# Performance work log

Hardware: AMD Instinct MI355X
Metric: run time of the kernel (lower is better)

## Reference

```python
import jax, jax.numpy as jnp
import numpy as np

EPS = 1e-06

def rmsnorm(x, w):
    x32 = x.astype(jnp.float32)
    var = jnp.mean(x32 * x32, axis=-1, keepdims=True)
    return w * (x32 * jax.lax.rsqrt(var + EPS)).astype(x.dtype)

def setup_inputs() -> dict:
    B, T, C = 16, 256, 16
    token_dim, text_dim = 1024, 512
    key = jax.random.key(0)
    ks = jax.random.split(key, 8)
    token_embeds = jax.random.normal(ks[0], (B, T, token_dim), dtype=jnp.float32)
    char_embeds = jax.random.normal(ks[1], (B, T, C, text_dim), dtype=jnp.float32)
    filler_embed = jax.random.normal(ks[2], (text_dim,), dtype=jnp.float32)
    mask = jax.random.randint(ks[3], (B, T, C), 0, 2).astype(bool)
    mask = mask.at[0].set(True)  # force max valid count == T*C (static output shape)
    token_ids_mask = jnp.ones((B, T), dtype=bool)
    # xavier-uniform-ish weights
    def xav(k, fan_out, fan_in, gain=1.0):
        lim = gain * np.sqrt(6.0 / (fan_in + fan_out))
        return jax.random.uniform(k, (fan_out, fan_in), jnp.float32, -lim, lim)
    W_down = xav(ks[4], text_dim, token_dim)
    W_proj = xav(ks[5], 3, text_dim, gain=0.2)
    W_fusion = xav(ks[6], text_dim, text_dim)
    w_pre = jnp.ones((token_dim,), jnp.float32)
    w_tok = jnp.ones((text_dim,), jnp.float32)
    w_char = jnp.ones((text_dim,), jnp.float32)
    return {"token_embeds": token_embeds, "token_ids_mask": token_ids_mask,
            "char_embeds": char_embeds, "char_ids_mask": mask,
            "filler_embed": filler_embed, "w_pre": w_pre, "w_tok": w_tok,
            "w_char": w_char, "W_down": W_down, "W_proj": W_proj,
            "W_fusion": W_fusion, "max_valid_chars": T * C}

def reference(token_embeds, token_ids_mask, char_embeds, char_ids_mask,
              filler_embed, w_pre, w_tok, w_char, W_down, W_proj, W_fusion,
              max_valid_chars):
    B, T, C, d = char_embeds.shape
    MV = int(max_valid_chars)
    tok = rmsnorm(token_embeds, w_pre)                       # [B,T,token_dim]
    feats = rmsnorm(jnp.einsum('btk,dk->btd', tok, W_down), w_tok)  # [B,T,d]
    params = jnp.einsum('btd,pd->btp', jax.nn.silu(feats), W_proj)  # [B,T,3]
    scale = params[..., 0][:, :, None, None]                 # [B,T,1,1]
    shift = params[..., 1][:, :, None, None]
    gate = jax.nn.sigmoid(params[..., 2][:, :, None, None])
    cn = rmsnorm(char_embeds, w_char)                        # [B,T,C,d]
    fused = jnp.einsum('btcd,ed->btce', jax.nn.silu(cn * (1.0 + scale) + shift), W_fusion)
    fused = gate * fused + (1.0 - gate) * cn                 # [B,T,C,d]
    flat = fused.reshape(B, T * C, d)
    m = char_ids_mask.reshape(B, T * C).astype(jnp.int32)
    pos = jnp.cumsum(m, axis=1) - 1                          # dest within row
    offs = jnp.arange(B, dtype=jnp.int32)[:, None] * MV
    idx = jnp.where(m > 0, offs + pos, B * MV)               # invalid -> dump slot
    buf = jnp.broadcast_to(filler_embed, (B * MV + 1, d))
    buf = buf.at[idx.reshape(-1)].set(flat.reshape(-1, d))
    return buf[: B * MV].reshape(B, MV, d)
```

## Files before the change

### kernel.cpp

```cpp
#include <hip/hip_runtime.h>
#include <cstdint>
#include <cstddef>

#define EPS 1e-6f

typedef short bf16x8 __attribute__((ext_vector_type(8)));
typedef float f32x4  __attribute__((ext_vector_type(4)));

__device__ __forceinline__ short f2bf(float x) {
    uint32_t u = __builtin_bit_cast(uint32_t, x);
    return (short)((u + 0x7FFFu + ((u >> 16) & 1u)) >> 16);
}

__global__ __launch_bounds__(256) void k_front(
    const void* __restrict__ maskp, int* __restrict__ v_list, int* __restrict__ counts,
    const float* __restrict__ Wf, short* __restrict__ Wfbf,
    const float* __restrict__ Wd, short* __restrict__ Wdbf,
    const float* __restrict__ tokens, const float* __restrict__ w_pre,
    short* __restrict__ tokbf) {
    const int blk = blockIdx.x, tid = threadIdx.x;
    if (blk < 16) {
        __shared__ int wtot[4], woff[4];
        __shared__ int mode_s;
        const int b = blk, lane = tid & 63, wave = tid >> 6;
        if (tid == 0) mode_s = 0;
        __syncthreads();
        {
            int bad = 0;
#pragma unroll
            for (int q = 0; q < 4; ++q)
                bad |= (((const uint32_t*)maskp)[q * 256 + tid] > 1u) ? 1 : 0;
            if (bad) mode_s = 1;
        }
        __syncthreads();
        int f[16];
        if (mode_s) {
            const uint4 v = ((const uint4*)maskp)[(b << 8) + tid];
            const uint32_t ws[4] = {v.x, v.y, v.z, v.w};
#pragma unroll
            for (int q = 0; q < 4; ++q) {
                f[q * 4 + 0] = (ws[q] & 0x000000ffu) != 0;
                f[q * 4 + 1] = (ws[q] & 0x0000ff00u) != 0;
                f[q * 4 + 2] = (ws[q] & 0x00ff0000u) != 0;
                f[q * 4 + 3] = (ws[q] & 0xff000000u) != 0;
            }
        } else {
            const uint4* mp = (const uint4*)maskp + ((size_t)b << 10) + tid * 4;
#pragma unroll
            for (int q = 0; q < 4; ++q) {
                const uint4 v = mp[q];
                f[q * 4 + 0] = v.x != 0; f[q * 4 + 1] = v.y != 0;
                f[q * 4 + 2] = v.z != 0; f[q * 4 + 3] = v.w != 0;
            }
        }
        int c = 0;
#pragma unroll
        for (int q = 0; q < 16; ++q) c += f[q];
        int incl = c;
#pragma unroll
        for (int off = 1; off < 64; off <<= 1) {
            const int n = __shfl_up(incl, off);
            if (lane >= off) incl += n;
        }
        if (lane == 63) wtot[wave] = incl;
        __syncthreads();
        if (tid == 0) {
            int run = 0;
#pragma unroll
            for (int wv = 0; wv < 4; ++wv) { woff[wv] = run; run += wtot[wv]; }
            counts[b] = run;
        }
        __syncthreads();
        int base = woff[wave] + incl - c;
        int* vl = v_list + (b << 12);
        const int i0 = tid * 16;
#pragma unroll
        for (int q = 0; q < 16; ++q)
            if (f[q]) vl[base++] = i0 + q;
    } else if (blk < 784) {
        const int gid = (blk - 16) * 256 + tid;
        const float* s; short* d; int i;
        if (gid < 65536) { s = Wf; d = Wfbf; i = gid; }
        else             { s = Wd; d = Wdbf; i = gid - 65536; }
        const float4 v = ((const float4*)s)[i];
        short4 o;
        o.x = f2bf(v.x); o.y = f2bf(v.y); o.z = f2bf(v.z); o.w = f2bf(v.w);
        ((short4*)d)[i] = o;
    } else {
        const int lane = tid & 63, wave = tid >> 6;
        const int row = (blk - 784) * 4 + wave;
        const float* xp = tokens + (size_t)row * 1024 + lane * 16;
        float4 x[4];
#pragma unroll
        for (int q = 0; q < 4; ++q) x[q] = *(const float4*)&xp[q * 4];
        float ss = 0.f;
#pragma unroll
        for (int q = 0; q < 4; ++q)
            ss += x[q].x * x[q].x + x[q].y * x[q].y + x[q].z * x[q].z + x[q].w * x[q].w;
#pragma unroll
        for (int off = 32; off > 0; off >>= 1) ss += __shfl_down(ss, off);
        ss = __shfl(ss, 0);
        const float r = rsqrtf(ss * (1.0f / 1024.0f) + EPS);
        const float* wp = w_pre + lane * 16;
        short* op = tokbf + (size_t)row * 1024 + lane * 16;
#pragma unroll
        for (int h = 0; h < 2; ++h) {
            bf16x8 o;
#pragma unroll
            for (int q = 0; q < 2; ++q) {
                const float4 wv = *(const float4*)&wp[h * 8 + q * 4];
                const float4 xv = x[h * 2 + q];
                o[q * 4 + 0] = f2bf(xv.x * wv.x * r);
                o[q * 4 + 1] = f2bf(xv.y * wv.y * r);
                o[q * 4 + 2] = f2bf(xv.z * wv.z * r);
                o[q * 4 + 3] = f2bf(xv.w * wv.w * r);
            }
            *(bf16x8*)&op[h * 8] = o;
        }
    }
}

__global__ __launch_bounds__(256) void k_gemm_tok(const short* __restrict__ tokbf,
                                                  const short* __restrict__ Wdbf,
                                                  float* __restrict__ feats) {
    __shared__ short As[128 * 32];
    __shared__ short Bs[128 * 32];
    const int tid = threadIdx.x, lane = tid & 63, w = tid >> 6;
    const int kt = blockIdx.x >> 7;
    const int mt = (blockIdx.x >> 2) & 31, nt = blockIdx.x & 3;
    const int wm = w >> 1, wn = w & 1;
    const int kbase = kt * 512;
    const short* hA = tokbf + (size_t)mt * 128 * 1024;
    const short* wB = Wdbf + (size_t)nt * 128 * 1024;

    f32x4 acc[4][4];
#pragma unroll
    for (int mi = 0; mi < 4; ++mi)
#pragma unroll
        for (int ni = 0; ni < 4; ++ni) acc[mi][ni] = (f32x4)0.f;

    const int rA = lane & 15, ch = lane >> 4;
    for (int kk = 0; kk < 512; kk += 32) {
#pragma unroll
        for (int q = 0; q < 2; ++q) {
            const int cid = (w * 2 + q) * 64 + lane;
            const int r = cid >> 2, kc = cid & 3;
            const int kcs = kc ^ ((r >> 1) & 3);
            const size_t go = (size_t)r * 1024 + kbase + kk + kcs * 8;
            __builtin_amdgcn_global_load_lds(
                (const __attribute__((address_space(1))) uint32_t*)(hA + go),
                (__attribute__((address_space(3))) uint32_t*)&As[(w * 2 + q) * 512], 16, 0, 0);
            __builtin_amdgcn_global_load_lds(
                (const __attribute__((address_space(1))) uint32_t*)(wB + go),
                (__attribute__((address_space(3))) uint32_t*)&Bs[(w * 2 + q) * 512], 16, 0, 0);
        }
        __syncthreads();
        bf16x8 af[4], bfr[4];
#pragma unroll
        for (int mi = 0; mi < 4; ++mi) {
            const int row = wm * 64 + mi * 16 + rA;
            af[mi] = *(const bf16x8*)&As[row * 32 + ((ch ^ ((row >> 1) & 3)) << 3)];
        }
#pragma unroll
        for (int ni = 0; ni < 4; ++ni) {
            const int row = wn * 64 + ni * 16 + rA;
            bfr[ni] = *(const bf16x8*)&Bs[row * 32 + ((ch ^ ((row >> 1) & 3)) << 3)];
        }
#pragma unroll
        for (int mi = 0; mi < 4; ++mi)
#pragma unroll
            for (int ni = 0; ni < 4; ++ni)
                acc[mi][ni] = __builtin_amdgcn_mfma_f32_16x16x32_bf16(af[mi], bfr[ni], acc[mi][ni], 0, 0, 0);
        __syncthreads();
    }
    float* fo = feats + (size_t)kt * 4096 * 512;
    const int rowb = mt * 128 + wm * 64 + (lane >> 4) * 4;
    const int colb = nt * 128 + wn * 64 + (lane & 15);
#pragma unroll
    for (int mi = 0; mi < 4; ++mi)
#pragma unroll
        for (int ni = 0; ni < 4; ++ni)
#pragma unroll
            for (int rg = 0; rg < 4; ++rg)
                fo[(size_t)(rowb + mi * 16 + rg) * 512 + colb + ni * 16] = acc[mi][ni][rg];
}

__global__ __launch_bounds__(64) void k_params(
    const float* __restrict__ feats_pre, const float* __restrict__ w_tok,
    const float* __restrict__ W_proj, float* __restrict__ params) {
    const int tk = blockIdx.x;
    const int lane = threadIdx.x;
    const int d0 = lane * 8;
    const float* fp0 = feats_pre + (size_t)tk * 512 + d0;
    const float* fp1 = fp0 + (size_t)4096 * 512;
    const float4 a0 = *(const float4*)&fp0[0];
    const float4 a1 = *(const float4*)&fp0[4];
    const float4 b0 = *(const float4*)&fp1[0];
    const float4 b1 = *(const float4*)&fp1[4];
    const float4 f0 = make_float4(a0.x + b0.x, a0.y + b0.y, a0.z + b0.z, a0.w + b0.w);
    const float4 f1 = make_float4(a1.x + b1.x, a1.y + b1.y, a1.z + b1.z, a1.w + b1.w);
    float ss = f0.x * f0.x + f0.y * f0.y + f0.z * f0.z + f0.w * f0.w
             + f1.x * f1.x + f1.y * f1.y + f1.z * f1.z + f1.w * f1.w;
#pragma unroll
    for (int off = 32; off > 0; off >>= 1) ss += __shfl_down(ss, off);
    ss = __shfl(ss, 0);
    const float rms = rsqrtf(ss * (1.0f / 512.0f) + EPS);

    const float4 wt0 = *(const float4*)&w_tok[d0];
    const float4 wt1 = *(const float4*)&w_tok[d0 + 4];
    float fv[8] = {f0.x, f0.y, f0.z, f0.w, f1.x, f1.y, f1.z, f1.w};
    float wv[8] = {wt0.x, wt0.y, wt0.z, wt0.w, wt1.x, wt1.y, wt1.z, wt1.w};
    float s[8];
#pragma unroll
    for (int j = 0; j < 8; ++j) {
        const float v = fv[j] * wv[j] * rms;
        s[j] = v / (1.0f + expf(-v));
    }
    float p[3];
#pragma unroll
    for (int q = 0; q < 3; ++q) {
        const float* Wp = W_proj + (size_t)q * 512 + d0;
        const float4 a = *(const float4*)&Wp[0];
        const float4 c = *(const float4*)&Wp[4];
        p[q] = s[0] * a.x + s[1] * a.y + s[2] * a.z + s[3] * a.w
             + s[4] * c.x + s[5] * c.y + s[6] * c.z + s[7] * c.w;
#pragma unroll
        for (int off = 32; off > 0; off >>= 1) p[q] += __shfl_down(p[q], off);
    }
    if (lane == 0) {
        float* po = params + (size_t)tk * 4;
        po[0] = 1.0f + p[0];
        po[1] = p[1];
        po[2] = 1.0f / (1.0f + expf(-p[2]));
        po[3] = 0.f;
    }
}

__global__ __launch_bounds__(256) void k_prep(
    const float* __restrict__ chars, const float* __restrict__ w_char,
    const float* __restrict__ params, const int* __restrict__ v_list,
    const int* __restrict__ counts, short* __restrict__ hb,
    float* __restrict__ rms_l, float* __restrict__ g_l) {
    const int tid = threadIdx.x, lane = tid & 63, wave = tid >> 6;
    const int b = blockIdx.x >> 10;
    const int j = (blockIdx.x & 1023) * 4 + wave;
    const int cnt = counts[b];
    const int cpad = (cnt + 127) & ~127;
    if (j >= cpad) return;
    short* hrow = hb + ((size_t)(b << 12) + j) * 512 + lane * 8;
    if (j >= cnt) {
        *(bf16x8*)hrow = (bf16x8)0;
        return;
    }
    const int i = v_list[(b << 12) + j];
    const float* xp = chars + ((size_t)(b << 12) + i) * 512 + lane * 8;
    const float4 x0 = *(const float4*)&xp[0];
    const float4 x1 = *(const float4*)&xp[4];
    float ss = x0.x * x0.x + x0.y * x0.y + x0.z * x0.z + x0.w * x0.w
             + x1.x * x1.x + x1.y * x1.y + x1.z * x1.z + x1.w * x1.w;
#pragma unroll
    for (int off = 32; off > 0; off >>= 1) ss += __shfl_down(ss, off);
    ss = __shfl(ss, 0);
    const float rms = rsqrtf(ss * (1.0f / 512.0f) + EPS);
    const float* pp = params + (size_t)((b << 8) + (i >> 4)) * 4;
    const float s1 = pp[0], sh = pp[1], g = pp[2];
    const float4 w0 = *(const float4*)&w_char[lane * 8];
    const float4 w1 = *(const float4*)&w_char[lane * 8 + 4];
    float xv[8] = {x0.x, x0.y, x0.z, x0.w, x1.x, x1.y, x1.z, x1.w};
    float wv[8] = {w0.x, w0.y, w0.z, w0.w, w1.x, w1.y, w1.z, w1.w};
    bf16x8 o;
#pragma unroll
    for (int q = 0; q < 8; ++q) {
        const float cn = wv[q] * xv[q] * rms;
        const float a = cn * s1 + sh;
        o[q] = f2bf(a / (1.0f + expf(-a)));
    }
    *(bf16x8*)hrow = o;
    if (lane == 0) {
        rms_l[(b << 12) + j] = rms;
        g_l[(b << 12) + j] = g;
    }
}

__global__ __launch_bounds__(256) void k_gemm_fus(
    const short* __restrict__ hb, const short* __restrict__ Wbf,
    const float* __restrict__ chars, const float* __restrict__ w_char,
    const float* __restrict__ rms_l, const float* __restrict__ g_l,
    const int* __restrict__ v_list, const int* __restrict__ counts,
    const float* __restrict__ filler, float* __restrict__ out) {
    const int wg = (blockIdx.x & 7) * 256 + (blockIdx.x >> 3);
    const int b = wg >> 7;
    const int mt = (wg >> 2) & 31;
    const int nt = wg & 3;
    const int tid = threadIdx.x, lane = tid & 63, w = tid >> 6;
    const int cnt = counts[b];
    const int row0 = mt * 128;
    if (row0 >= cnt) {
        const int colb0 = nt * 128;
        const f32x4 f = *(const f32x4*)(filler + colb0 + (tid & 31) * 4);
        float* o0 = out + ((size_t)(b << 12) + row0) * 512 + colb0 + (tid & 31) * 4;
        for (int r = tid >> 5; r < 128; r += 8)
            __builtin_nontemporal_store(f, (f32x4*)&o0[(size_t)r * 512]);
        return;
    }

    __shared__ short As[128 * 32];
    __shared__ short Bs[128 * 32];
    __shared__ float g_s[128], rms_s[128];
    __shared__ int idx_s[128];
    const int wm = w >> 1, wn = w & 1;

    if (tid < 128) {
        const int j = row0 + tid;
        const bool valid = j < cnt;
        idx_s[tid] = valid ? v_list[(b << 12) + j] : 0;
        g_s[tid]   = valid ? g_l[(b << 12) + j] : 0.f;
        rms_s[tid] = valid ? rms_l[(b << 12) + j] : 0.f;
    }

    const short* hA = hb + ((size_t)(b << 12) + row0) * 512;
    const short* wB = Wbf + (size_t)nt * 128 * 512;

    f32x4 acc[4][4];
#pragma unroll
    for (int mi = 0; mi < 4; ++mi)
#pragma unroll
        for (int ni = 0; ni < 4; ++ni) acc[mi][ni] = (f32x4)0.f;

    const int rA = lane & 15, ch = lane >> 4;
    for (int kk = 0; kk < 512; kk += 32) {
#pragma unroll
        for (int q = 0; q < 2; ++q) {
            const int cid = (w * 2 + q) * 64 + lane;
            const int r = cid >> 2, kc = cid & 3;
            const int kcs = kc ^ ((r >> 1) & 3);
            const size_t go = (size_t)r * 512 + kk + kcs * 8;
            __builtin_amdgcn_global_load_lds(
                (const __attribute__((address_space(1))) uint32_t*)(hA + go),
                (__attribute__((address_space(3))) uint32_t*)&As[(w * 2 + q) * 512], 16, 0, 0);
            __builtin_amdgcn_global_load_lds(
                (const __attribute__((address_space(1))) uint32_t*)(wB + go),
                (__attribute__((address_space(3))) uint32_t*)&Bs[(w * 2 + q) * 512], 16, 0, 0);
        }
        __syncthreads();
        bf16x8 af[4], bfr[4];
#pragma unroll
        for (int mi = 0; mi < 4; ++mi) {
            const int row = wm * 64 + mi * 16 + rA;
            af[mi] = *(const bf16x8*)&As[row * 32 + ((ch ^ ((row >> 1) & 3)) << 3)];
        }
#pragma unroll
        for (int ni = 0; ni < 4; ++ni) {
            const int row = wn * 64 + ni * 16 + rA;
            bfr[ni] = *(const bf16x8*)&Bs[row * 32 + ((ch ^ ((row >> 1) & 3)) << 3)];
        }
#pragma unroll
        for (int mi = 0; mi < 4; ++mi)
#pragma unroll
            for (int ni = 0; ni < 4; ++ni)
                acc[mi][ni] = __builtin_amdgcn_mfma_f32_16x16x32_bf16(af[mi], bfr[ni], acc[mi][ni], 0, 0, 0);
        __syncthreads();
    }

    const int colb = nt * 128 + wn * 64 + (lane & 15);
    float wcv[4];
#pragma unroll
    for (int ni = 0; ni < 4; ++ni) wcv[ni] = w_char[colb + ni * 16];
#pragma unroll
    for (int mi = 0; mi < 4; ++mi) {
#pragma unroll
        for (int rg = 0; rg < 4; ++rg) {
            const int jl = wm * 64 + mi * 16 + (lane >> 4) * 4 + rg;
            const int j = row0 + jl;
            const size_t orow = ((size_t)(b << 12) + j) * 512;
            if (j < cnt) {
                const float g = g_s[jl], rm = rms_s[jl];
                const size_t xrow = ((size_t)(b << 12) + idx_s[jl]) * 512;
#pragma unroll
                for (int ni = 0; ni < 4; ++ni) {
                    const int col = colb + ni * 16;
                    const float x = chars[xrow + col];
                    const float cn = wcv[ni] * x * rm;
                    __builtin_nontemporal_store(g * acc[mi][ni][rg] + (1.0f - g) * cn,
                                                &out[orow + col]);
                }
            } else {
#pragma unroll
                for (int ni = 0; ni < 4; ++ni) {
                    const int col = colb + ni * 16;
                    __builtin_nontemporal_store(filler[col], &out[orow + col]);
                }
            }
        }
    }
}

extern "C" void kernel_launch(void* const* d_in, const int* in_sizes, int n_in,
                              void* d_out, int out_size, void* d_ws, size_t ws_size,
                              hipStream_t stream) {
    const float* tokens = (const float*)d_in[0];
    const float* chars  = (const float*)d_in[2];
    const void*  cmask  = d_in[3];
    const float* filler = (const float*)d_in[4];
    const float* w_pre  = (const float*)d_in[5];
    const float* w_tok  = (const float*)d_in[6];
    const float* w_char = (const float*)d_in[7];
    const float* W_down = (const float*)d_in[8];
    const float* W_proj = (const float*)d_in[9];
    const float* W_fus  = (const float*)d_in[10];
    float* out = (float*)d_out;

    float* feats_pre = (float*)d_ws;
    float* params    = feats_pre + (size_t)2 * 4096 * 512;
    int*   counts    = (int*)(params + (size_t)4096 * 4);
    int*   v_list    = counts + 16;
    float* rms_l     = (float*)(v_list + 65536);
    float* g_l       = rms_l + 65536;
    short* Wbf       = (short*)(g_l + 65536);
    short* hb        = Wbf + (size_t)512 * 512;
    short* tokbf     = hb + (size_t)16 * 4096 * 512;
    short* Wdbf      = tokbf + (size_t)4096 * 1024;

    k_front<<<1808, 256, 0, stream>>>(cmask, v_list, counts, W_fus, Wbf,
                                      W_down, Wdbf, tokens, w_pre, tokbf);
    k_gemm_tok<<<256, 256, 0, stream>>>(tokbf, Wdbf, feats_pre);
    k_params<<<4096, 64, 0, stream>>>(feats_pre, w_tok, W_proj, params);
    k_prep<<<16384, 256, 0, stream>>>(chars, w_char, params, v_list, counts, hb, rms_l, g_l);
    k_gemm_fus<<<2048, 256, 0, stream>>>(hb, Wbf, chars, w_char, rms_l, g_l,
                                         v_list, counts, filler, out);
}
```

Baseline: 326.3 us.

## Double-buffer LDS tiles in both GEMMs and use regular output stores

Both bf16 MFMA GEMM kernels now keep two LDS buffers and issue the global-to-LDS loads for the next K-slice before running MFMAs on the current one. This halves the barrier count per K step and aims to overlap memory latency with compute. Separately, the output and filler writes in the fusion kernel switch from nontemporal stores to ordinary stores. The extra LDS doubles shared memory per block, which may reduce occupancy.

```diff
diff --git a/kernel.cpp b/kernel.cpp
--- a/kernel.cpp
+++ b/kernel.cpp
@@ -123,8 +123,8 @@
 __global__ __launch_bounds__(256) void k_gemm_tok(const short* __restrict__ tokbf,
                                                   const short* __restrict__ Wdbf,
                                                   float* __restrict__ feats) {
-    __shared__ short As[128 * 32];
-    __shared__ short Bs[128 * 32];
+    __shared__ short As[2][128 * 32];
+    __shared__ short Bs[2][128 * 32];
     const int tid = threadIdx.x, lane = tid & 63, w = tid >> 6;
     const int kt = blockIdx.x >> 7;
     const int mt = (blockIdx.x >> 2) & 31, nt = blockIdx.x & 3;
@@ -140,39 +140,52 @@
         for (int ni = 0; ni < 4; ++ni) acc[mi][ni] = (f32x4)0.f;
 
     const int rA = lane & 15, ch = lane >> 4;
-    for (int kk = 0; kk < 512; kk += 32) {
+
+    auto STAGE = [&](int bufi, int kk) {
 #pragma unroll
         for (int q = 0; q < 2; ++q) {
             const int cid = (w * 2 + q) * 64 + lane;
             const int r = cid >> 2, kc = cid & 3;
             const int kcs = kc ^ ((r >> 1) & 3);
-            const size_t go = (size_t)r * 1024 + kbase + kk + kcs * 8;
+            const size_t go = (size_t)r * 1024 + kk + kcs * 8;
             __builtin_amdgcn_global_load_lds(
                 (const __attribute__((address_space(1))) uint32_t*)(hA + go),
-                (__attribute__((address_space(3))) uint32_t*)&As[(w * 2 + q) * 512], 16, 0, 0);
+                (__attribute__((address_space(3))) uint32_t*)&As[bufi][(w * 2 + q) * 512], 16, 0, 0);
             __builtin_amdgcn_global_load_lds(
                 (const __attribute__((address_space(1))) uint32_t*)(wB + go),
-                (__attribute__((address_space(3))) uint32_t*)&Bs[(w * 2 + q) * 512], 16, 0, 0);
-        }
-        __syncthreads();
+                (__attribute__((address_space(3))) uint32_t*)&Bs[bufi][(w * 2 + q) * 512], 16, 0, 0);
+        }
+    };
+    auto COMPUTE = [&](int bufi) {
         bf16x8 af[4], bfr[4];
 #pragma unroll
         for (int mi = 0; mi < 4; ++mi) {
             const int row = wm * 64 + mi * 16 + rA;
-            af[mi] = *(const bf16x8*)&As[row * 32 + ((ch ^ ((row >> 1) & 3)) << 3)];
+            af[mi] = *(const bf16x8*)&As[bufi][row * 32 + ((ch ^ ((row >> 1) & 3)) << 3)];
         }
 #pragma unroll
         for (int ni = 0; ni < 4; ++ni) {
             const int row = wn * 64 + ni * 16 + rA;
-            bfr[ni] = *(const bf16x8*)&Bs[row * 32 + ((ch ^ ((row >> 1) & 3)) << 3)];
+            bfr[ni] = *(const bf16x8*)&Bs[bufi][row * 32 + ((ch ^ ((row >> 1) & 3)) << 3)];
         }
 #pragma unroll
         for (int mi = 0; mi < 4; ++mi)
 #pragma unroll
             for (int ni = 0; ni < 4; ++ni)
                 acc[mi][ni] = __builtin_amdgcn_mfma_f32_16x16x32_bf16(af[mi], bfr[ni], acc[mi][ni], 0, 0, 0);
-        __syncthreads();
-    }
+    };
+
+    STAGE(0, kbase);
+    __syncthreads();
+    for (int kk = 0; kk < 512; kk += 64) {
+        STAGE(1, kbase + kk + 32);
+        COMPUTE(0);
+        __syncthreads();
+        if (kk + 64 < 512) STAGE(0, kbase + kk + 64);
+        COMPUTE(1);
+        __syncthreads();
+    }
+
     float* fo = feats + (size_t)kt * 4096 * 512;
     const int rowb = mt * 128 + wm * 64 + (lane >> 4) * 4;
     const int colb = nt * 128 + wn * 64 + (lane & 15);
@@ -297,15 +310,15 @@
     const int row0 = mt * 128;
     if (row0 >= cnt) {
         const int colb0 = nt * 128;
-        const f32x4 f = *(const f32x4*)(filler + colb0 + (tid & 31) * 4);
+        const float4 f = *(const float4*)(filler + colb0 + (tid & 31) * 4);
         float* o0 = out + ((size_t)(b << 12) + row0) * 512 + colb0 + (tid & 31) * 4;
         for (int r = tid >> 5; r < 128; r += 8)
-            __builtin_nontemporal_store(f, (f32x4*)&o0[(size_t)r * 512]);
+            *(float4*)&o0[(size_t)r * 512] = f;
         return;
     }
 
-    __shared__ short As[128 * 32];
-    __shared__ short Bs[128 * 32];
+    __shared__ short As[2][128 * 32];
+    __shared__ short Bs[2][128 * 32];
     __shared__ float g_s[128], rms_s[128];
     __shared__ int idx_s[128];
     const int wm = w >> 1, wn = w & 1;
@@ -328,7 +341,8 @@
         for (int ni = 0; ni < 4; ++ni) acc[mi][ni] = (f32x4)0.f;
 
     const int rA = lane & 15, ch = lane >> 4;
-    for (int kk = 0; kk < 512; kk += 32) {
+
+    auto STAGE = [&](int bufi, int kk) {
 #pragma unroll
         for (int q = 0; q < 2; ++q) {
             const int cid = (w * 2 + q) * 64 + lane;
@@ -337,28 +351,39 @@
             const size_t go = (size_t)r * 512 + kk + kcs * 8;
             __builtin_amdgcn_global_load_lds(
                 (const __attribute__((address_space(1))) uint32_t*)(hA + go),
-                (__attribute__((address_space(3))) uint32_t*)&As[(w * 2 + q) * 512], 16, 0, 0);
+                (__attribute__((address_space(3))) uint32_t*)&As[bufi][(w * 2 + q) * 512], 16, 0, 0);
             __builtin_amdgcn_global_load_lds(
                 (const __attribute__((address_space(1))) uint32_t*)(wB + go),
-                (__attribute__((address_space(3))) uint32_t*)&Bs[(w * 2 + q) * 512], 16, 0, 0);
-        }
-        __syncthreads();
+                (__attribute__((address_space(3))) uint32_t*)&Bs[bufi][(w * 2 + q) * 512], 16, 0, 0);
+        }
+    };
+    auto COMPUTE = [&](int bufi) {
         bf16x8 af[4], bfr[4];
 #pragma unroll
         for (int mi = 0; mi < 4; ++mi) {
             const int row = wm * 64 + mi * 16 + rA;
-            af[mi] = *(const bf16x8*)&As[row * 32 + ((ch ^ ((row >> 1) & 3)) << 3)];
+            af[mi] = *(const bf16x8*)&As[bufi][row * 32 + ((ch ^ ((row >> 1) & 3)) << 3)];
         }
 #pragma unroll
         for (int ni = 0; ni < 4; ++ni) {
             const int row = wn * 64 + ni * 16 + rA;
-            bfr[ni] = *(const bf16x8*)&Bs[row * 32 + ((ch ^ ((row >> 1) & 3)) << 3)];
+            bfr[ni] = *(const bf16x8*)&Bs[bufi][row * 32 + ((ch ^ ((row >> 1) & 3)) << 3)];
         }
 #pragma unroll
         for (int mi = 0; mi < 4; ++mi)
 #pragma unroll
             for (int ni = 0; ni < 4; ++ni)
                 acc[mi][ni] = __builtin_amdgcn_mfma_f32_16x16x32_bf16(af[mi], bfr[ni], acc[mi][ni], 0, 0, 0);
+    };
+
+    STAGE(0, 0);
+    __syncthreads();
+    for (int kk = 0; kk < 512; kk += 64) {
+        STAGE(1, kk + 32);
+        COMPUTE(0);
+        __syncthreads();
+        if (kk + 64 < 512) STAGE(0, kk + 64);
+        COMPUTE(1);
         __syncthreads();
     }
 
@@ -381,14 +406,13 @@
                     const int col = colb + ni * 16;
                     const float x = chars[xrow + col];
                     const float cn = wcv[ni] * x * rm;
-                    __builtin_nontemporal_store(g * acc[mi][ni][rg] + (1.0f - g) * cn,
-                                                &out[orow + col]);
+                    out[orow + col] = g * acc[mi][ni][rg] + (1.0f - g) * cn;
                 }
             } else {
 #pragma unroll
                 for (int ni = 0; ni < 4; ++ni) {
                     const int col = colb + ni * 16;
-                    __builtin_nontemporal_store(filler[col], &out[orow + col]);
+                    out[orow + col] = filler[col];
                 }
             }
         }
```

Measured after the change: 340.3 us. 1.04x slower.
